# Kernel tuning notes

Measured on AMD Instinct MI355X. Metric: run time of the kernel, lower is better.

The kernel has to match this reference:

```python
import jax, jax.numpy as jnp
import numpy as np

EMBED_DIM = 768
NUM_HEADS = 12
HEAD_DIM = EMBED_DIM // NUM_HEADS


def setup_inputs() -> dict:
    key = jax.random.key(0)
    ks = jax.random.split(key, 9)
    d = EMBED_DIM
    s = 1.0 / np.sqrt(d)
    x = jax.random.normal(ks[0], (1, 4096, d), dtype=jnp.float32)
    # nn.Linear weights stored as [out, in]; init ~ U(-1/sqrt(in), 1/sqrt(in))
    wq = jax.random.uniform(ks[1], (d, d), jnp.float32, -s, s)
    bq = jax.random.uniform(ks[2], (d,), jnp.float32, -s, s)
    wk = jax.random.uniform(ks[3], (d, d), jnp.float32, -s, s)
    bk = jax.random.uniform(ks[4], (d,), jnp.float32, -s, s)
    wv = jax.random.uniform(ks[5], (d, d), jnp.float32, -s, s)
    bv = jax.random.uniform(ks[6], (d,), jnp.float32, -s, s)
    ww = jax.random.uniform(ks[7], (d, d), jnp.float32, -s, s)
    bw = jax.random.uniform(ks[8], (d,), jnp.float32, -s, s)
    return {"x": x, "wq": wq, "bq": bq, "wk": wk, "bk": bk,
            "wv": wv, "bv": bv, "ww": ww, "bw": bw}


def reference(x, wq, bq, wk, bk, wv, bv, ww, bw):
    B, S, D = x.shape
    H, Hd = NUM_HEADS, HEAD_DIM
    # Linear: x @ W^T + b, then split heads -> [B, H, S, Hd]
    def proj(w, b):
        y = x @ w.T + b
        return y.reshape(B, S, H, Hd).transpose(0, 2, 1, 3)
    q = proj(wq, bq)
    k = proj(wk, bk)
    v = proj(wv, bv)
    scores = jnp.einsum('bhqd,bhkd->bhqk', q, k) / jnp.sqrt(jnp.float32(Hd))
    attn = jax.nn.softmax(scores, axis=-1)
    out = jnp.einsum('bhqk,bhkd->bhqd', attn, v)  # [B,H,S,Hd]
    out = out.transpose(0, 2, 1, 3).reshape(B, S, D)
    return out @ ww.T + bw
```

## Files before the change

kernel.cpp:

```cpp
#include <hip/hip_runtime.h>
#include <cstdio>


using u16 = unsigned short;
typedef __bf16 bf16x8 __attribute__((ext_vector_type(8)));
typedef float f32x4 __attribute__((ext_vector_type(4)));
typedef float f32x16 __attribute__((ext_vector_type(16)));
typedef unsigned int u32x4 __attribute__((ext_vector_type(4)));
typedef u16 u16x4 __attribute__((ext_vector_type(4)));

constexpr int SEQ = 4096;
constexpr int DIM = 768;
constexpr int NH = 12;
constexpr int HD = 64;
constexpr int LDT = 72;
constexpr int LDM = 68;
constexpr float SM_PRE = 0.18033688011112042f;
constexpr float DEFER_THR = 8.0f;

__device__ __forceinline__ u16 f2bf(float f) {
  union { float f; unsigned u; } v{f};
  unsigned r = v.u + 0x7fffu + ((v.u >> 16) & 1u);
  return (u16)(r >> 16);
}
__device__ __forceinline__ unsigned cvtpk_bf16(float a, float b) {
  unsigned r;
  asm("v_cvt_pk_bf16_f32 %0, %1, %2" : "=v"(r) : "v"(a), "v"(b));
  return r;
}
__device__ __forceinline__ void swap32(unsigned& a, unsigned& b) {
  asm volatile("v_permlane32_swap_b32 %0, %1" : "+v"(a), "+v"(b));
}
__device__ __forceinline__ bf16x8 bc16(const u16* p) {
  return __builtin_bit_cast(bf16x8, *(const u32x4*)p);
}

__global__ __launch_bounds__(256) void prep_all(const float* __restrict__ x,
                                                const float* __restrict__ wq,
                                                const float* __restrict__ wk,
                                                const float* __restrict__ wv,
                                                u16* __restrict__ xb,
                                                u16* __restrict__ wqb,
                                                u16* __restrict__ wkb,
                                                u16* __restrict__ wvb) {
  constexpr size_t NX = (size_t)SEQ * DIM, NW = (size_t)DIM * DIM;
  size_t i = ((size_t)blockIdx.x * 256 + threadIdx.x) * 8;
  const float* src;
  u16* dst;
  size_t off;
  if (i < NX) { src = x; dst = xb; off = i; }
  else if (i < NX + NW) { src = wq; dst = wqb; off = i - NX; }
  else if (i < NX + 2 * NW) { src = wk; dst = wkb; off = i - NX - 2 * NW + NW; }
  else { src = wv; dst = wvb; off = i - NX - 3 * NW + NW; }
  float4 f0 = *(const float4*)(src + off);
  float4 f1 = *(const float4*)(src + off + 4);
  u32x4 w = {cvtpk_bf16(f0.x, f0.y), cvtpk_bf16(f0.z, f0.w),
             cvtpk_bf16(f1.x, f1.y), cvtpk_bf16(f1.z, f1.w)};
  *(u32x4*)(dst + off) = w;
}

__global__ __launch_bounds__(256) void prep_one(const float* __restrict__ w,
                                                u16* __restrict__ wb) {
  size_t off = ((size_t)blockIdx.x * 256 + threadIdx.x) * 8;
  float4 f0 = *(const float4*)(w + off);
  float4 f1 = *(const float4*)(w + off + 4);
  u32x4 v = {cvtpk_bf16(f0.x, f0.y), cvtpk_bf16(f0.z, f0.w),
             cvtpk_bf16(f1.x, f1.y), cvtpk_bf16(f1.z, f1.w)};
  *(u32x4*)(wb + off) = v;
}

__global__ __launch_bounds__(256) void qkv_gemm(const u16* __restrict__ xb,
                                                const u16* __restrict__ wqb,
                                                const u16* __restrict__ wkb,
                                                const u16* __restrict__ wvb,
                                                const float* __restrict__ bq,
                                                const float* __restrict__ bk,
                                                const float* __restrict__ bv,
                                                u16* __restrict__ Qb,
                                                u16* __restrict__ Kb,
                                                u16* __restrict__ Vtb) {
  __shared__ alignas(16) u16 As[64 * LDT];
  __shared__ alignas(16) u16 Bq[64 * LDT];
  __shared__ alignas(16) u16 Bk[64 * LDT];
  __shared__ alignas(16) u16 Bv[64 * LDT];

  const int tid = threadIdx.x, lane = tid & 63, wave = tid >> 6;
  const int lg = lane >> 4, ln = lane & 15;
  const int bid = blockIdx.x;
  const int swz = (bid & 7) * 96 + (bid >> 3);
  const int mt = swz / 12, nt = swz % 12;
  const int m0 = mt * 64, n0 = nt * 64;
  const int sr = tid >> 2, sc = (tid & 3) * 16;

  f32x4 acc[4][3] = {};

  for (int kk = 0; kk < DIM; kk += 64) {
    {
      const u32x4* s = (const u32x4*)(xb + (size_t)(m0 + sr) * DIM + kk + sc);
      *(u32x4*)&As[sr * LDT + sc] = s[0];
      *(u32x4*)&As[sr * LDT + sc + 8] = s[1];
    }
    {
      const u32x4* s = (const u32x4*)(wqb + (size_t)(n0 + sr) * DIM + kk + sc);
      *(u32x4*)&Bq[sr * LDT + sc] = s[0];
      *(u32x4*)&Bq[sr * LDT + sc + 8] = s[1];
    }
    {
      const u32x4* s = (const u32x4*)(wkb + (size_t)(n0 + sr) * DIM + kk + sc);
      *(u32x4*)&Bk[sr * LDT + sc] = s[0];
      *(u32x4*)&Bk[sr * LDT + sc + 8] = s[1];
    }
    {
      const u32x4* s = (const u32x4*)(wvb + (size_t)(n0 + sr) * DIM + kk + sc);
      *(u32x4*)&Bv[sr * LDT + sc] = s[0];
      *(u32x4*)&Bv[sr * LDT + sc + 8] = s[1];
    }
    __syncthreads();

#pragma unroll
    for (int c = 0; c < 2; ++c) {
      const int k0 = c * 32 + lg * 8;
      bf16x8 a[4];
#pragma unroll
      for (int i = 0; i < 4; ++i)
        a[i] = bc16(&As[(i * 16 + ln) * LDT + k0]);
      {
        bf16x8 b = bc16(&Bq[(wave * 16 + ln) * LDT + k0]);
#pragma unroll
        for (int i = 0; i < 4; ++i)
          acc[i][0] = __builtin_amdgcn_mfma_f32_16x16x32_bf16(a[i], b, acc[i][0], 0, 0, 0);
      }
      {
        bf16x8 b = bc16(&Bk[(wave * 16 + ln) * LDT + k0]);
#pragma unroll
        for (int i = 0; i < 4; ++i)
          acc[i][1] = __builtin_amdgcn_mfma_f32_16x16x32_bf16(a[i], b, acc[i][1], 0, 0, 0);
      }
      {
        bf16x8 b = bc16(&Bv[(wave * 16 + ln) * LDT + k0]);
#pragma unroll
        for (int i = 0; i < 4; ++i)
          acc[i][2] = __builtin_amdgcn_mfma_f32_16x16x32_bf16(a[i], b, acc[i][2], 0, 0, 0);
      }
    }
    __syncthreads();
  }

  const int col = n0 + wave * 16 + ln;
  const float bvq = bq[col], bvk = bk[col], bvv = bv[col];
#pragma unroll
  for (int i = 0; i < 4; ++i) {
    const int rowb = m0 + i * 16 + lg * 4;
#pragma unroll
    for (int r = 0; r < 4; ++r) {
      Qb[(size_t)(rowb + r) * DIM + col] = f2bf((acc[i][0][r] + bvq) * SM_PRE);
      Kb[(size_t)(rowb + r) * DIM + col] = f2bf(acc[i][1][r] + bvk);
    }
    u16x4 pk;
#pragma unroll
    for (int r = 0; r < 4; ++r) pk[r] = f2bf(acc[i][2][r] + bvv);
    *(u16x4*)&Vtb[(size_t)col * SEQ + rowb] = pk;
  }
}

__global__ __launch_bounds__(256) void out_gemm(const u16* __restrict__ Ab,
                                                const u16* __restrict__ Wb,
                                                const float* __restrict__ bias,
                                                float* __restrict__ out) {
  __shared__ alignas(16) u16 As[64 * LDT];
  __shared__ alignas(16) u16 Bs[64 * LDT];

  const int tid = threadIdx.x, lane = tid & 63, wave = tid >> 6;
  const int lg = lane >> 4, ln = lane & 15;
  const int bid = blockIdx.x;
  const int swz = (bid & 7) * 96 + (bid >> 3);
  const int mt = swz / 12, nt = swz % 12;
  const int m0 = mt * 64, n0 = nt * 64;
  const int sr = tid >> 2, sc = (tid & 3) * 16;

  f32x4 acc[4] = {};

  for (int kk = 0; kk < DIM; kk += 64) {
    {
      const u32x4* s = (const u32x4*)(Ab + (size_t)(m0 + sr) * DIM + kk + sc);
      *(u32x4*)&As[sr * LDT + sc] = s[0];
      *(u32x4*)&As[sr * LDT + sc + 8] = s[1];
    }
    {
      const u32x4* s = (const u32x4*)(Wb + (size_t)(n0 + sr) * DIM + kk + sc);
      *(u32x4*)&Bs[sr * LDT + sc] = s[0];
      *(u32x4*)&Bs[sr * LDT + sc + 8] = s[1];
    }
    __syncthreads();
#pragma unroll
    for (int c = 0; c < 2; ++c) {
      const int k0 = c * 32 + lg * 8;
      bf16x8 a = bc16(&As[(wave * 16 + ln) * LDT + k0]);
#pragma unroll
      for (int j = 0; j < 4; ++j) {
        bf16x8 b = bc16(&Bs[(j * 16 + ln) * LDT + k0]);
        acc[j] = __builtin_amdgcn_mfma_f32_16x16x32_bf16(a, b, acc[j], 0, 0, 0);
      }
    }
    __syncthreads();
  }

  const int rowb = m0 + wave * 16 + lg * 4;
#pragma unroll
  for (int j = 0; j < 4; ++j) {
    const int col = n0 + j * 16 + ln;
    const float bv = bias[col];
#pragma unroll
    for (int r = 0; r < 4; ++r) out[(size_t)(rowb + r) * DIM + col] = acc[j][r] + bv;
  }
}

__global__ __launch_bounds__(256, 3) void attn_kernel(const u16* __restrict__ Q,
                                                      const u16* __restrict__ K,
                                                      const u16* __restrict__ Vt,
                                                      u16* __restrict__ AO) {
  __shared__ alignas(16) u16 Ks[2][64 * LDT];
  __shared__ alignas(16) u16 Vs[2][64 * LDT];
  __shared__ float sm[4][32], sl[4][32];

  const int tid = threadIdx.x, lane = tid & 63, wave = tid >> 6;
  const int l31 = lane & 31, hi = lane >> 5;
  const int g = wave >> 1, p = wave & 1;
  const int bid = blockIdx.x;
  const int swz = (bid & 7) * 96 + (bid >> 3);
  const int h = swz >> 6;
  const int q0 = (swz & 63) * 64;
  const int qw = q0 + g * 32;

  bf16x8 qf[4];
#pragma unroll
  for (int c = 0; c < 4; ++c)
    qf[c] = bc16(Q + (size_t)(qw + l31) * DIM + h * HD + c * 16 + hi * 8);

  float m_ = -1e30f, l_ = 0.f;
  f32x16 oacc[2] = {};

  const int srow = tid >> 2;
  const int scol = (tid & 3) * 16;

  const u16* Kh = K + (size_t)h * HD;
  const u16* Vh = Vt + (size_t)h * HD * SEQ;
  constexpr int NT = SEQ / 64;

  u32x4 kp0, kp1, vp0, vp1;
  auto pf = [&](int t) {
    const u32x4* s = (const u32x4*)(Kh + (size_t)(t * 64 + srow) * DIM + scol);
    kp0 = s[0]; kp1 = s[1];
    const u32x4* v = (const u32x4*)(Vh + (size_t)srow * SEQ + t * 64 + scol);
    vp0 = v[0]; vp1 = v[1];
  };
  auto stage = [&](int buf) {
    u16* kd = &Ks[buf][srow * LDT + scol];
    *(u32x4*)kd = kp0; *(u32x4*)(kd + 8) = kp1;
    u16* vd = &Vs[buf][srow * LDT + scol];
    *(u32x4*)vd = vp0; *(u32x4*)(vd + 8) = vp1;
  };

  pf(0);
  stage(0);
  pf(1);
  __syncthreads();

  auto round = [&](int t, int cur) {
    bf16x8 kf[4];
#pragma unroll
    for (int c = 0; c < 4; ++c)
      kf[c] = bc16(&Ks[cur][(p * 32 + l31) * LDT + c * 16 + hi * 8]);

    if (t + 1 < NT) {
      stage(cur ^ 1);
      pf(t + 2 < NT ? t + 2 : t + 1);
    }

    f32x16 st = {};
    __builtin_amdgcn_s_setprio(1);
#pragma unroll
    for (int c = 0; c < 4; ++c)
      st = __builtin_amdgcn_mfma_f32_32x32x16_bf16(kf[c], qf[c], st, 0, 0, 0);
    __builtin_amdgcn_s_setprio(0);

    float x0 = fmaxf(fmaxf(st[0], st[4]), fmaxf(st[8], st[12]));
    float x1 = fmaxf(fmaxf(st[1], st[5]), fmaxf(st[9], st[13]));
    float x2 = fmaxf(fmaxf(st[2], st[6]), fmaxf(st[10], st[14]));
    float x3 = fmaxf(fmaxf(st[3], st[7]), fmaxf(st[11], st[15]));
    float pm = fmaxf(fmaxf(x0, x1), fmaxf(x2, x3));
    pm = fmaxf(pm, __shfl_xor(pm, 32));

    if (__ballot(pm > m_ + DEFER_THR)) {
      const float mn = fmaxf(m_, pm);
      const float scl = __builtin_amdgcn_exp2f(m_ - mn);
      l_ *= scl;
      m_ = mn;
      float fac[16];
#pragma unroll
      for (int r = 0; r < 16; ++r)
        fac[r] = __shfl(scl, (r & 3) + 8 * (r >> 2) + 4 * hi);
#pragma unroll
      for (int nd = 0; nd < 2; ++nd)
#pragma unroll
        for (int r = 0; r < 16; ++r) oacc[nd][r] *= fac[r];
    }

#pragma unroll
    for (int r = 0; r < 16; ++r) st[r] = __builtin_amdgcn_exp2f(st[r] - m_);
    {
      float s0 = (st[0] + st[4]) + (st[8] + st[12]);
      float s1 = (st[1] + st[5]) + (st[9] + st[13]);
      float s2 = (st[2] + st[6]) + (st[10] + st[14]);
      float s3 = (st[3] + st[7]) + (st[11] + st[15]);
      float rs = (s0 + s1) + (s2 + s3);
      rs += __shfl_xor(rs, 32);
      l_ += rs;
    }

    unsigned c0 = cvtpk_bf16(st[0], st[1]), c1 = cvtpk_bf16(st[2], st[3]);
    unsigned c2 = cvtpk_bf16(st[4], st[5]), c3 = cvtpk_bf16(st[6], st[7]);
    unsigned c4 = cvtpk_bf16(st[8], st[9]), c5 = cvtpk_bf16(st[10], st[11]);
    unsigned c6 = cvtpk_bf16(st[12], st[13]), c7 = cvtpk_bf16(st[14], st[15]);
    swap32(c0, c2); swap32(c1, c3); swap32(c4, c6); swap32(c5, c7);
    bf16x8 pa0 = __builtin_bit_cast(bf16x8, u32x4{c0, c1, c2, c3});
    bf16x8 pa1 = __builtin_bit_cast(bf16x8, u32x4{c4, c5, c6, c7});

    __builtin_amdgcn_s_setprio(1);
#pragma unroll
    for (int nd = 0; nd < 2; ++nd) {
      const int vrow = (nd * 32 + l31) * LDT + p * 32;
      bf16x8 vA = bc16(&Vs[cur][vrow + hi * 8]);
      oacc[nd] = __builtin_amdgcn_mfma_f32_32x32x16_bf16(pa0, vA, oacc[nd], 0, 0, 0);
      bf16x8 vB = bc16(&Vs[cur][vrow + 16 + hi * 8]);
      oacc[nd] = __builtin_amdgcn_mfma_f32_32x32x16_bf16(pa1, vB, oacc[nd], 0, 0, 0);
    }
    __builtin_amdgcn_s_setprio(0);
    __syncthreads();
  };

  for (int t = 0; t < NT; t += 2) {
    round(t, 0);
    round(t + 1, 1);
  }

  if (hi == 0) { sm[wave][l31] = m_; sl[wave][l31] = l_; }
  __syncthreads();

  const float m0s = sm[g * 2][l31], m1s = sm[g * 2 + 1][l31];
  const float l0s = sl[g * 2][l31], l1s = sl[g * 2 + 1][l31];
  const float M = fmaxf(m0s, m1s);
  const float L = l0s * __builtin_amdgcn_exp2f(m0s - M) +
                  l1s * __builtin_amdgcn_exp2f(m1s - M);
  const float fac = __builtin_amdgcn_exp2f(m_ - M);
  const float Linv = 1.f / L;
  float facr[16], Lr[16];
#pragma unroll
  for (int r = 0; r < 16; ++r) {
    const int ri = (r & 3) + 8 * (r >> 2) + 4 * hi;
    facr[r] = __shfl(fac, ri);
    Lr[r] = __shfl(Linv, ri);
  }

  float* Om = (float*)Ks;
  if (p == 1) {
#pragma unroll
    for (int nd = 0; nd < 2; ++nd)
#pragma unroll
      for (int r = 0; r < 16; ++r) {
        const int row = (r & 3) + 8 * (r >> 2) + 4 * hi;
        Om[(g * 32 + row) * LDM + nd * 32 + l31] = oacc[nd][r] * facr[r];
      }
  }
  __syncthreads();
  if (p == 0) {
#pragma unroll
    for (int nd = 0; nd < 2; ++nd)
#pragma unroll
      for (int r = 0; r < 16; ++r) {
        const int row = (r & 3) + 8 * (r >> 2) + 4 * hi;
        const float v = (oacc[nd][r] * facr[r] +
                         Om[(g * 32 + row) * LDM + nd * 32 + l31]) * Lr[r];
        AO[(size_t)(qw + row) * DIM + h * HD + nd * 32 + l31] = f2bf(v);
      }
  }
}

extern "C" void kernel_launch(void* const* d_in, const int* in_sizes, int n_in,
                              void* d_out, int out_size, void* d_ws, size_t ws_size,
                              hipStream_t stream) {
  const float* x = (const float*)d_in[0];
  const float* wq = (const float*)d_in[1];
  const float* bq = (const float*)d_in[2];
  const float* wk = (const float*)d_in[3];
  const float* bk = (const float*)d_in[4];
  const float* wv = (const float*)d_in[5];
  const float* bv = (const float*)d_in[6];
  const float* ww = (const float*)d_in[7];
  const float* bw = (const float*)d_in[8];

  const size_t mat = (size_t)SEQ * DIM;
  const size_t nw = (size_t)DIM * DIM;
  if (ws_size < 4 * mat * sizeof(u16)) {
    fprintf(stderr, "kernel_launch: ws too small (%zu)\n", ws_size);
    return;
  }
  u16* Qb = (u16*)d_ws;
  u16* Kb = Qb + mat;
  u16* Vtb = Kb + mat;
  u16* AOb = Vtb + mat;
  u16* xb = AOb;
  u16* wqb = (u16*)d_out;
  u16* wkb = wqb + nw;
  u16* wvb = wkb + nw;
  u16* wwb = Kb;

  prep_all<<<dim3(2400), dim3(256), 0, stream>>>(x, wq, wk, wv, xb, wqb, wkb, wvb);
  qkv_gemm<<<dim3(768), dim3(256), 0, stream>>>(xb, wqb, wkb, wvb, bq, bk, bv, Qb, Kb, Vtb);
  attn_kernel<<<dim3(768), dim3(256), 0, stream>>>(Qb, Kb, Vtb, AOb);
  prep_one<<<dim3(288), dim3(256), 0, stream>>>(ww, wwb);
  out_gemm<<<dim3(768), dim3(256), 0, stream>>>(AOb, wwb, bw, (float*)d_out);
}
```

Baseline: 134.8 us.

## Double-buffer projection GEMMs with register prefetch and hoist V fragment loads

The QKV and output projection GEMMs switch from single-buffered 64-wide K tiles to double-buffered 32-wide K tiles. The next tile is prefetched into registers and staged to LDS while the MFMAs run, leaving one barrier per step. The output GEMM also swaps its A/B fragment roles so each wave loads one weight fragment per step. In attention, all V fragments are read from LDS before the K/V staging, and the row max uses a 3-input max tree, which adds register pressure.

```diff
diff --git a/kernel.cpp b/kernel.cpp
--- a/kernel.cpp
+++ b/kernel.cpp
@@ -14,6 +14,7 @@
 constexpr int NH = 12;
 constexpr int HD = 64;
 constexpr int LDT = 72;
+constexpr int LDA2 = 40;
 constexpr int LDM = 68;
 constexpr float SM_PRE = 0.18033688011112042f;
 constexpr float DEFER_THR = 8.0f;
@@ -33,6 +34,9 @@
 }
 __device__ __forceinline__ bf16x8 bc16(const u16* p) {
   return __builtin_bit_cast(bf16x8, *(const u32x4*)p);
+}
+__device__ __forceinline__ float fmax3(float a, float b, float c) {
+  return fmaxf(fmaxf(a, b), c);
 }
 
 __global__ __launch_bounds__(256) void prep_all(const float* __restrict__ x,
@@ -79,10 +83,10 @@
                                                 u16* __restrict__ Qb,
                                                 u16* __restrict__ Kb,
                                                 u16* __restrict__ Vtb) {
-  __shared__ alignas(16) u16 As[64 * LDT];
-  __shared__ alignas(16) u16 Bq[64 * LDT];
-  __shared__ alignas(16) u16 Bk[64 * LDT];
-  __shared__ alignas(16) u16 Bv[64 * LDT];
+  __shared__ alignas(16) u16 As[2][64 * LDA2];
+  __shared__ alignas(16) u16 Bq[2][64 * LDA2];
+  __shared__ alignas(16) u16 Bk[2][64 * LDA2];
+  __shared__ alignas(16) u16 Bv[2][64 * LDA2];
 
   const int tid = threadIdx.x, lane = tid & 63, wave = tid >> 6;
   const int lg = lane >> 4, ln = lane & 15;
@@ -90,58 +94,48 @@
   const int swz = (bid & 7) * 96 + (bid >> 3);
   const int mt = swz / 12, nt = swz % 12;
   const int m0 = mt * 64, n0 = nt * 64;
-  const int sr = tid >> 2, sc = (tid & 3) * 16;
+  const int srow = tid >> 2, scol = (tid & 3) * 8;
 
   f32x4 acc[4][3] = {};
 
-  for (int kk = 0; kk < DIM; kk += 64) {
-    {
-      const u32x4* s = (const u32x4*)(xb + (size_t)(m0 + sr) * DIM + kk + sc);
-      *(u32x4*)&As[sr * LDT + sc] = s[0];
-      *(u32x4*)&As[sr * LDT + sc + 8] = s[1];
-    }
-    {
-      const u32x4* s = (const u32x4*)(wqb + (size_t)(n0 + sr) * DIM + kk + sc);
-      *(u32x4*)&Bq[sr * LDT + sc] = s[0];
-      *(u32x4*)&Bq[sr * LDT + sc + 8] = s[1];
-    }
-    {
-      const u32x4* s = (const u32x4*)(wkb + (size_t)(n0 + sr) * DIM + kk + sc);
-      *(u32x4*)&Bk[sr * LDT + sc] = s[0];
-      *(u32x4*)&Bk[sr * LDT + sc + 8] = s[1];
-    }
-    {
-      const u32x4* s = (const u32x4*)(wvb + (size_t)(n0 + sr) * DIM + kk + sc);
-      *(u32x4*)&Bv[sr * LDT + sc] = s[0];
-      *(u32x4*)&Bv[sr * LDT + sc + 8] = s[1];
-    }
-    __syncthreads();
-
-#pragma unroll
-    for (int c = 0; c < 2; ++c) {
-      const int k0 = c * 32 + lg * 8;
-      bf16x8 a[4];
-#pragma unroll
-      for (int i = 0; i < 4; ++i)
-        a[i] = bc16(&As[(i * 16 + ln) * LDT + k0]);
-      {
-        bf16x8 b = bc16(&Bq[(wave * 16 + ln) * LDT + k0]);
-#pragma unroll
-        for (int i = 0; i < 4; ++i)
-          acc[i][0] = __builtin_amdgcn_mfma_f32_16x16x32_bf16(a[i], b, acc[i][0], 0, 0, 0);
-      }
-      {
-        bf16x8 b = bc16(&Bk[(wave * 16 + ln) * LDT + k0]);
-#pragma unroll
-        for (int i = 0; i < 4; ++i)
-          acc[i][1] = __builtin_amdgcn_mfma_f32_16x16x32_bf16(a[i], b, acc[i][1], 0, 0, 0);
-      }
-      {
-        bf16x8 b = bc16(&Bv[(wave * 16 + ln) * LDT + k0]);
-#pragma unroll
-        for (int i = 0; i < 4; ++i)
-          acc[i][2] = __builtin_amdgcn_mfma_f32_16x16x32_bf16(a[i], b, acc[i][2], 0, 0, 0);
-      }
+  u32x4 pA, pQ, pK, pV;
+  auto pf = [&](int kk) {
+    pA = *(const u32x4*)(xb + (size_t)(m0 + srow) * DIM + kk + scol);
+    pQ = *(const u32x4*)(wqb + (size_t)(n0 + srow) * DIM + kk + scol);
+    pK = *(const u32x4*)(wkb + (size_t)(n0 + srow) * DIM + kk + scol);
+    pV = *(const u32x4*)(wvb + (size_t)(n0 + srow) * DIM + kk + scol);
+  };
+  auto stage = [&](int b) {
+    *(u32x4*)&As[b][srow * LDA2 + scol] = pA;
+    *(u32x4*)&Bq[b][srow * LDA2 + scol] = pQ;
+    *(u32x4*)&Bk[b][srow * LDA2 + scol] = pK;
+    *(u32x4*)&Bv[b][srow * LDA2 + scol] = pV;
+  };
+
+  constexpr int NS = DIM / 32;
+  pf(0);
+  stage(0);
+  pf(32);
+  __syncthreads();
+
+  for (int s = 0; s < NS; ++s) {
+    const int cur = s & 1;
+    bf16x8 a[4];
+#pragma unroll
+    for (int i = 0; i < 4; ++i)
+      a[i] = bc16(&As[cur][(i * 16 + ln) * LDA2 + lg * 8]);
+    bf16x8 fq = bc16(&Bq[cur][(wave * 16 + ln) * LDA2 + lg * 8]);
+    bf16x8 fk = bc16(&Bk[cur][(wave * 16 + ln) * LDA2 + lg * 8]);
+    bf16x8 fv = bc16(&Bv[cur][(wave * 16 + ln) * LDA2 + lg * 8]);
+    if (s + 1 < NS) {
+      stage(cur ^ 1);
+      if (s + 2 < NS) pf((s + 2) * 32);
+    }
+#pragma unroll
+    for (int i = 0; i < 4; ++i) {
+      acc[i][0] = __builtin_amdgcn_mfma_f32_16x16x32_bf16(a[i], fq, acc[i][0], 0, 0, 0);
+      acc[i][1] = __builtin_amdgcn_mfma_f32_16x16x32_bf16(a[i], fk, acc[i][1], 0, 0, 0);
+      acc[i][2] = __builtin_amdgcn_mfma_f32_16x16x32_bf16(a[i], fv, acc[i][2], 0, 0, 0);
     }
     __syncthreads();
   }
@@ -167,8 +161,8 @@
                                                 const u16* __restrict__ Wb,
                                                 const float* __restrict__ bias,
                                                 float* __restrict__ out) {
-  __shared__ alignas(16) u16 As[64 * LDT];
-  __shared__ alignas(16) u16 Bs[64 * LDT];
+  __shared__ alignas(16) u16 As[2][64 * LDA2];
+  __shared__ alignas(16) u16 Bs[2][64 * LDA2];
 
   const int tid = threadIdx.x, lane = tid & 63, wave = tid >> 6;
   const int lg = lane >> 4, ln = lane & 15;
@@ -176,40 +170,48 @@
   const int swz = (bid & 7) * 96 + (bid >> 3);
   const int mt = swz / 12, nt = swz % 12;
   const int m0 = mt * 64, n0 = nt * 64;
-  const int sr = tid >> 2, sc = (tid & 3) * 16;
+  const int srow = tid >> 2, scol = (tid & 3) * 8;
 
   f32x4 acc[4] = {};
 
-  for (int kk = 0; kk < DIM; kk += 64) {
-    {
-      const u32x4* s = (const u32x4*)(Ab + (size_t)(m0 + sr) * DIM + kk + sc);
-      *(u32x4*)&As[sr * LDT + sc] = s[0];
-      *(u32x4*)&As[sr * LDT + sc + 8] = s[1];
-    }
-    {
-      const u32x4* s = (const u32x4*)(Wb + (size_t)(n0 + sr) * DIM + kk + sc);
-      *(u32x4*)&Bs[sr * LDT + sc] = s[0];
-      *(u32x4*)&Bs[sr * LDT + sc + 8] = s[1];
-    }
+  u32x4 pA, pB;
+  auto pf = [&](int kk) {
+    pA = *(const u32x4*)(Ab + (size_t)(m0 + srow) * DIM + kk + scol);
+    pB = *(const u32x4*)(Wb + (size_t)(n0 + srow) * DIM + kk + scol);
+  };
+  auto stage = [&](int b) {
+    *(u32x4*)&As[b][srow * LDA2 + scol] = pA;
+    *(u32x4*)&Bs[b][srow * LDA2 + scol] = pB;
+  };
+
+  constexpr int NS = DIM / 32;
+  pf(0);
+  stage(0);
+  pf(32);
+  __syncthreads();
+
+  for (int s = 0; s < NS; ++s) {
+    const int cur = s & 1;
+    bf16x8 b = bc16(&Bs[cur][(wave * 16 + ln) * LDA2 + lg * 8]);
+    bf16x8 a[4];
+#pragma unroll
+    for (int j = 0; j < 4; ++j)
+      a[j] = bc16(&As[cur][(j * 16 + ln) * LDA2 + lg * 8]);
+    if (s + 1 < NS) {
+      stage(cur ^ 1);
+      if (s + 2 < NS) pf((s + 2) * 32);
+    }
+#pragma unroll
+    for (int j = 0; j < 4; ++j)
+      acc[j] = __builtin_amdgcn_mfma_f32_16x16x32_bf16(a[j], b, acc[j], 0, 0, 0);
     __syncthreads();
-#pragma unroll
-    for (int c = 0; c < 2; ++c) {
-      const int k0 = c * 32 + lg * 8;
-      bf16x8 a = bc16(&As[(wave * 16 + ln) * LDT + k0]);
-#pragma unroll
-      for (int j = 0; j < 4; ++j) {
-        bf16x8 b = bc16(&Bs[(j * 16 + ln) * LDT + k0]);
-        acc[j] = __builtin_amdgcn_mfma_f32_16x16x32_bf16(a, b, acc[j], 0, 0, 0);
-      }
-    }
-    __syncthreads();
-  }
-
-  const int rowb = m0 + wave * 16 + lg * 4;
+  }
+
+  const int col = n0 + wave * 16 + ln;
+  const float bv = bias[col];
 #pragma unroll
   for (int j = 0; j < 4; ++j) {
-    const int col = n0 + j * 16 + ln;
-    const float bv = bias[col];
+    const int rowb = m0 + j * 16 + lg * 4;
 #pragma unroll
     for (int r = 0; r < 4; ++r) out[(size_t)(rowb + r) * DIM + col] = acc[j][r] + bv;
   }
@@ -267,10 +269,16 @@
   __syncthreads();
 
   auto round = [&](int t, int cur) {
-    bf16x8 kf[4];
-#pragma unroll
-    for (int c = 0; c < 4; ++c)
-      kf[c] = bc16(&Ks[cur][(p * 32 + l31) * LDT + c * 16 + hi * 8]);
+    bf16x8 kf0 = bc16(&Ks[cur][(p * 32 + l31) * LDT + 0 * 16 + hi * 8]);
+    bf16x8 kf1 = bc16(&Ks[cur][(p * 32 + l31) * LDT + 1 * 16 + hi * 8]);
+    bf16x8 kf2 = bc16(&Ks[cur][(p * 32 + l31) * LDT + 2 * 16 + hi * 8]);
+    bf16x8 kf3 = bc16(&Ks[cur][(p * 32 + l31) * LDT + 3 * 16 + hi * 8]);
+    const int vr0 = (0 * 32 + l31) * LDT + p * 32;
+    const int vr1 = (1 * 32 + l31) * LDT + p * 32;
+    bf16x8 vf00 = bc16(&Vs[cur][vr0 + hi * 8]);
+    bf16x8 vf01 = bc16(&Vs[cur][vr0 + 16 + hi * 8]);
+    bf16x8 vf10 = bc16(&Vs[cur][vr1 + hi * 8]);
+    bf16x8 vf11 = bc16(&Vs[cur][vr1 + 16 + hi * 8]);
 
     if (t + 1 < NT) {
       stage(cur ^ 1);
@@ -279,16 +287,18 @@
 
     f32x16 st = {};
     __builtin_amdgcn_s_setprio(1);
-#pragma unroll
-    for (int c = 0; c < 4; ++c)
-      st = __builtin_amdgcn_mfma_f32_32x32x16_bf16(kf[c], qf[c], st, 0, 0, 0);
+    st = __builtin_amdgcn_mfma_f32_32x32x16_bf16(kf0, qf[0], st, 0, 0, 0);
+    st = __builtin_amdgcn_mfma_f32_32x32x16_bf16(kf1, qf[1], st, 0, 0, 0);
+    st = __builtin_amdgcn_mfma_f32_32x32x16_bf16(kf2, qf[2], st, 0, 0, 0);
+    st = __builtin_amdgcn_mfma_f32_32x32x16_bf16(kf3, qf[3], st, 0, 0, 0);
     __builtin_amdgcn_s_setprio(0);
 
-    float x0 = fmaxf(fmaxf(st[0], st[4]), fmaxf(st[8], st[12]));
-    float x1 = fmaxf(fmaxf(st[1], st[5]), fmaxf(st[9], st[13]));
-    float x2 = fmaxf(fmaxf(st[2], st[6]), fmaxf(st[10], st[14]));
-    float x3 = fmaxf(fmaxf(st[3], st[7]), fmaxf(st[11], st[15]));
-    float pm = fmaxf(fmaxf(x0, x1), fmaxf(x2, x3));
+    float g0 = fmax3(st[0], st[4], st[8]);
+    float g1 = fmax3(st[12], st[1], st[5]);
+    float g2 = fmax3(st[9], st[13], st[2]);
+    float g3 = fmax3(st[6], st[10], st[14]);
+    float g4 = fmax3(st[3], st[7], st[11]);
+    float pm = fmaxf(fmax3(g0, g1, g2), fmax3(g3, g4, st[15]));
     pm = fmaxf(pm, __shfl_xor(pm, 32));
 
     if (__ballot(pm > m_ + DEFER_THR)) {
@@ -327,14 +337,10 @@
     bf16x8 pa1 = __builtin_bit_cast(bf16x8, u32x4{c4, c5, c6, c7});
 
     __builtin_amdgcn_s_setprio(1);
-#pragma unroll
-    for (int nd = 0; nd < 2; ++nd) {
-      const int vrow = (nd * 32 + l31) * LDT + p * 32;
-      bf16x8 vA = bc16(&Vs[cur][vrow + hi * 8]);
-      oacc[nd] = __builtin_amdgcn_mfma_f32_32x32x16_bf16(pa0, vA, oacc[nd], 0, 0, 0);
-      bf16x8 vB = bc16(&Vs[cur][vrow + 16 + hi * 8]);
-      oacc[nd] = __builtin_amdgcn_mfma_f32_32x32x16_bf16(pa1, vB, oacc[nd], 0, 0, 0);
-    }
+    oacc[0] = __builtin_amdgcn_mfma_f32_32x32x16_bf16(pa0, vf00, oacc[0], 0, 0, 0);
+    oacc[0] = __builtin_amdgcn_mfma_f32_32x32x16_bf16(pa1, vf01, oacc[0], 0, 0, 0);
+    oacc[1] = __builtin_amdgcn_mfma_f32_32x32x16_bf16(pa0, vf10, oacc[1], 0, 0, 0);
+    oacc[1] = __builtin_amdgcn_mfma_f32_32x32x16_bf16(pa1, vf11, oacc[1], 0, 0, 0);
     __builtin_amdgcn_s_setprio(0);
     __syncthreads();
   };
```

New measurement: 131.5 us. 1.03x faster.
